# Kernel optimization log

Hardware: AMD Instinct MI355X
Metric: run time of the kernel (lower is better)

The kernel has to match this reference:

```python
import jax, jax.numpy as jnp
import numpy as np

N_NODES = 30000
N_EDGES = 150000
N_REL = 10
IN_DIM = 256
OUT_DIM = 256


def setup_inputs() -> dict:
    key = jax.random.key(0)
    ks = jax.random.split(key, 10)
    s = 1.0 / np.sqrt(IN_DIM)  # ~nn.Linear init scale
    return {
        "x": jax.random.normal(ks[0], (N_NODES, IN_DIM), jnp.float32),
        "W_self": jax.random.uniform(ks[1], (IN_DIM, OUT_DIM), jnp.float32, -s, s),
        "b_self": jax.random.uniform(ks[2], (OUT_DIM,), jnp.float32, -s, s),
        "W_fwd": jax.random.uniform(ks[3], (N_REL, IN_DIM, OUT_DIM), jnp.float32, -s, s),
        "b_fwd": jax.random.uniform(ks[4], (N_REL, OUT_DIM), jnp.float32, -s, s),
        "W_rev": jax.random.uniform(ks[5], (N_REL, IN_DIM, OUT_DIM), jnp.float32, -s, s),
        "b_rev": jax.random.uniform(ks[6], (N_REL, OUT_DIM), jnp.float32, -s, s),
        "dep_idx": jax.random.randint(ks[7], (N_EDGES,), 0, N_NODES, jnp.int32),
        "rel_idx": jax.random.randint(ks[8], (N_EDGES,), 0, N_REL, jnp.int32),
        "gov_idx": jax.random.randint(ks[9], (N_EDGES,), 0, N_NODES, jnp.int32),
    }


def reference(x, W_self, b_self, W_fwd, b_fwd, W_rev, b_rev, dep_idx, rel_idx, gov_idx):
    # self transform for every token: [N, out]
    out = x @ W_self + b_self
    # transform all nodes by every relation weight up-front: [R, N, out]
    H_fwd = jnp.einsum("ni,rio->rno", x, W_fwd) + b_fwd[:, None, :]
    H_rev = jnp.einsum("ni,rio->rno", x, W_rev) + b_rev[:, None, :]
    # per-edge gather: forward msg uses governor feature, reverse msg uses dependent
    msg_fwd = H_fwd[rel_idx, gov_idx]  # [E, out]
    msg_rev = H_rev[rel_idx, dep_idx]  # [E, out]
    # scatter-add: forward msg -> dependent, reverse msg -> governor
    out = out.at[dep_idx].add(msg_fwd)
    out = out.at[gov_idx].add(msg_rev)
    return out
```

## Files before the change

### kernel.cpp

```cpp
#include <hip/hip_runtime.h>

#define N_NODES 30000
#define N_EDGES 150000
#define N_REL 10
#define DIM 256

#define SORT_BLOCKS 120
#define SORT_CHUNK ((N_EDGES + SORT_BLOCKS - 1) / SORT_BLOCKS)

#define SCAN_CHUNK 256
#define SCAN_BLOCKS ((N_NODES + SCAN_CHUNK - 1) / SCAN_CHUNK)

#define PREP_XB 7500
#define PREP_WT 1344

typedef __attribute__((ext_vector_type(8))) short bf16x8;
typedef __attribute__((ext_vector_type(4))) float f32x4;

__device__ __forceinline__ unsigned short f2bf(float f) {
  union { float f; unsigned int u; } v; v.f = f;
  unsigned int u = v.u;
  unsigned int r = u + 0x7fffu + ((u >> 16) & 1u);
  return (unsigned short)(r >> 16);
}


__global__ void prep_hist_kernel(const float* __restrict__ x,
                                 const float* __restrict__ Wf,
                                 const float* __restrict__ Wr,
                                 const float* __restrict__ Ws,
                                 const int* __restrict__ rel,
                                 const int* __restrict__ dep,
                                 const int* __restrict__ gov,
                                 unsigned short* __restrict__ xbf,
                                 unsigned short* __restrict__ wt,
                                 int* __restrict__ block_counts,
                                 int* __restrict__ cnt) {
  int b = blockIdx.x;
  if (b < PREP_XB) {
    int idx = b * 256 + threadIdx.x;
    float4 v = reinterpret_cast<const float4*>(x)[idx];
    ushort4 o;
    o.x = f2bf(v.x); o.y = f2bf(v.y); o.z = f2bf(v.z); o.w = f2bf(v.w);
    reinterpret_cast<ushort4*>(xbf)[idx] = o;
  } else if (b < PREP_XB + PREP_WT) {
    int wb = b - PREP_XB;
    int bb = wb >> 6;
    int tile = wb & 63;
    int ib = tile >> 3, ob = tile & 7;
    const float* src = (bb < N_REL) ? (Wf + (size_t)bb * 65536)
                     : (bb < 2 * N_REL) ? (Wr + (size_t)(bb - N_REL) * 65536)
                     : Ws;
    __shared__ unsigned short tile_s[32][33];
    int c = threadIdx.x & 31, r0 = threadIdx.x >> 5;
    #pragma unroll
    for (int k = 0; k < 4; ++k) {
      int rr = r0 + k * 8;
      tile_s[rr][c] = f2bf(src[(ib * 32 + rr) * 256 + ob * 32 + c]);
    }
    __syncthreads();
    #pragma unroll
    for (int k = 0; k < 4; ++k) {
      int rr = r0 + k * 8;
      wt[(size_t)bb * 65536 + (ob * 32 + rr) * 256 + ib * 32 + c] =
          tile_s[c][rr];
    }
  } else {
    int hb = b - PREP_XB - PREP_WT;
    __shared__ int h[N_REL];
    if (threadIdx.x < N_REL) h[threadIdx.x] = 0;
    __syncthreads();
    int beg = hb * SORT_CHUNK;
    int end = min(beg + SORT_CHUNK, N_EDGES);
    for (int e = beg + threadIdx.x; e < end; e += blockDim.x) {
      atomicAdd(&h[rel[e]], 1);
      atomicAdd(&cnt[dep[e]], 1);
      atomicAdd(&cnt[N_NODES + gov[e]], 1);
    }
    __syncthreads();
    if (threadIdx.x < N_REL)
      block_counts[hb * N_REL + threadIdx.x] = h[threadIdx.x];
  }
}


__global__ void scanA_kernel(const int* __restrict__ cnt,
                             int* __restrict__ tmp, int* __restrict__ sums) {
  __shared__ int s[SCAN_CHUNK];
  int d = blockIdx.y, b = blockIdx.x, t = threadIdx.x;
  int i = b * SCAN_CHUNK + t;
  int v = (i < N_NODES) ? cnt[d * N_NODES + i] : 0;
  s[t] = v;
  __syncthreads();
  for (int off = 1; off < SCAN_CHUNK; off <<= 1) {
    int add = (t >= off) ? s[t - off] : 0;
    __syncthreads();
    s[t] += add;
    __syncthreads();
  }
  if (i < N_NODES) tmp[d * N_NODES + i] = s[t] - v;
  if (t == SCAN_CHUNK - 1) sums[d * SCAN_BLOCKS + b] = s[t];
}


__global__ void scan_finish_kernel(const int* __restrict__ sums,
                                   const int* __restrict__ tmp,
                                   const int* __restrict__ block_counts,
                                   int* __restrict__ rp,
                                   int* __restrict__ cursor,
                                   int* __restrict__ rel_start,
                                   int* __restrict__ block_offset) {
  int d = blockIdx.y, b = blockIdx.x, t = threadIdx.x;

  if (b == SCAN_BLOCKS) {
    if (d == 1) return;
    __shared__ int tot[N_REL];
    __shared__ int rstart[N_REL + 1];
    int r = t;
    if (r < N_REL) {
      int s = 0;
      for (int bb = 0; bb < SORT_BLOCKS; ++bb) s += block_counts[bb * N_REL + r];
      tot[r] = s;
    }
    __syncthreads();
    if (t == 0) {
      int s = 0;
      for (int i = 0; i < N_REL; ++i) { rstart[i] = s; s += tot[i]; }
      rstart[N_REL] = s;
      for (int i = 0; i <= N_REL; ++i) rel_start[i] = rstart[i];
    }
    __syncthreads();
    if (r < N_REL) {
      int run = rstart[r];
      for (int bb = 0; bb < SORT_BLOCKS; ++bb) {
        block_offset[bb * N_REL + r] = run;
        run += block_counts[bb * N_REL + r];
      }
    }
    return;
  }

  __shared__ int ssum[SCAN_BLOCKS];
  __shared__ int spre[SCAN_BLOCKS + 1];
  if (t < SCAN_BLOCKS) ssum[t] = sums[d * SCAN_BLOCKS + t];
  __syncthreads();
  if (t == 0) {
    int run = 0;
    for (int i = 0; i < SCAN_BLOCKS; ++i) { spre[i] = run; run += ssum[i]; }
    spre[SCAN_BLOCKS] = run;
  }
  __syncthreads();
  int chunk = spre[b];
  int i = b * SCAN_CHUNK + t;
  if (i < N_NODES) {
    int v = tmp[d * N_NODES + i] + chunk;
    rp[d * (N_NODES + 1) + i] = v;
    cursor[d * N_NODES + i] = v;
  }
  if (b == 0 && t == 0) rp[d * (N_NODES + 1) + N_NODES] = spre[SCAN_BLOCKS];
}


__global__ void scatter_all_kernel(const int* __restrict__ rel,
                                   const int* __restrict__ dep,
                                   const int* __restrict__ gov,
                                   const int* __restrict__ block_offset,
                                   int* __restrict__ cursor,
                                   int* __restrict__ perm,
                                   int* __restrict__ srcf,
                                   int* __restrict__ srcr,
                                   int* __restrict__ colf,
                                   int* __restrict__ colr) {
  __shared__ int cur[N_REL];
  if (threadIdx.x < N_REL)
    cur[threadIdx.x] = block_offset[blockIdx.x * N_REL + threadIdx.x];
  __syncthreads();
  int beg = blockIdx.x * SORT_CHUNK;
  int end = min(beg + SORT_CHUNK, N_EDGES);
  for (int e = beg + threadIdx.x; e < end; e += blockDim.x) {
    int dp = dep[e], gv = gov[e];
    int pos = atomicAdd(&cur[rel[e]], 1);
    perm[pos] = e;
    srcf[pos] = gv;
    srcr[pos] = dp;
    colf[atomicAdd(&cursor[dp], 1)] = pos;
    colr[atomicAdd(&cursor[N_NODES + gv], 1)] = pos;
  }
}


__global__ __launch_bounds__(256, 2)
void mega_gemm_kernel(const unsigned short* __restrict__ xbf,
                      const unsigned short* __restrict__ wt,
                      const float* __restrict__ b_self,
                      const float* __restrict__ b_fwd,
                      const float* __restrict__ b_rev,
                      const int* __restrict__ srcf,
                      const int* __restrict__ srcr,
                      const int* __restrict__ rel_start,
                      unsigned short* __restrict__ msg,
                      float* __restrict__ out) {
  const int bkt = blockIdx.y;
  const bool is_self = (bkt >= 2 * N_REL);
  const bool fwd = bkt < N_REL;
  const int r = is_self ? 0 : (fwd ? bkt : bkt - N_REL);

  int beg, cnt;
  const int* src_arr = fwd ? srcf : srcr;
  unsigned short* mdir = msg + (fwd ? 0 : (size_t)N_EDGES * DIM);
  if (is_self) {
    beg = (bkt - 2 * N_REL) * (N_NODES / 2);
    cnt = N_NODES / 2;
  } else {
    beg = rel_start[r];
    cnt = rel_start[r + 1] - beg;
  }
  const int ntiles = (cnt + 63) >> 6;
  const int GX = gridDim.x;

  const int tid = threadIdx.x;
  const int wave = tid >> 6, lane = tid & 63;
  const int lm = lane & 15, q = lane >> 4;
  const int nb = wave * 64;
  const int half = lane >> 5;

  __shared__ int s_src[2][64];
  __shared__ unsigned short sA[2][64 * DIM];

  bf16x8 wf[8][4];
  const unsigned short* wbase =
      wt + (size_t)(is_self ? 2 * N_REL : bkt) * DIM * DIM;
  #pragma unroll
  for (int kk = 0; kk < 8; ++kk)
    #pragma unroll
    for (int ni = 0; ni < 4; ++ni)
      wf[kk][ni] = *reinterpret_cast<const bf16x8*>(
          wbase + (size_t)(nb + ni * 16 + lm) * DIM + kk * 32 + q * 8);

  const float* bptr = is_self ? b_self : ((fwd ? b_fwd : b_rev) + r * DIM);
  float bias[4];
  #pragma unroll
  for (int ni = 0; ni < 4; ++ni) bias[ni] = bptr[nb + ni * 16 + lm];

  int swz[8];
  #pragma unroll
  for (int i = 0; i < 8; ++i)
    swz[i] = (((lane & 31) ^ ((i * 2 + half) & 7)) * 8);
  int rowoff[4];
  #pragma unroll
  for (int mi = 0; mi < 4; ++mi) rowoff[mi] = (mi * 16 + lm) * DIM;
  int ckoff[8];
  #pragma unroll
  for (int kk = 0; kk < 8; ++kk)
    ckoff[kk] = ((kk * 4 + q) ^ (lm & 7)) * 8;

  int t = blockIdx.x;
  if (t >= ntiles) return;

  auto load_idx = [&](int tt) -> int {
    int tile0_ = tt << 6;
    if (is_self) {
      int rr = beg + tile0_ + tid;
      return rr < beg + cnt ? rr : beg + cnt - 1;
    } else {
      int p_ = tile0_ + tid;
      p_ = p_ < cnt ? p_ : cnt - 1;
      return src_arr[beg + p_];
    }
  };

  auto issue_stage = [&](int p) {
    const int* sp = s_src[p];
    unsigned short* db = sA[p];
    #pragma unroll
    for (int i = 0; i < 8; ++i) {
      int ldsrow = wave * 16 + i * 2;
      int rr = sp[ldsrow + half];
      const unsigned short* g = xbf + (size_t)rr * DIM + swz[i];
      __builtin_amdgcn_global_load_lds(
          (const __attribute__((address_space(1))) void*)g,
          (__attribute__((address_space(3))) void*)(db + ldsrow * DIM),
          16, 0, 0);
    }
  };

  auto step = [&](int cur) {
    const int tile0 = t << 6;
    const int rows_valid = min(64, cnt - tile0);
    const bool have_next = (t + GX) < ntiles;
    const bool have_next2 = (t + 2 * GX) < ntiles;

    __syncthreads();
    if (have_next) issue_stage(cur ^ 1);
    if (tid < 64 && have_next2) s_src[cur][tid] = load_idx(t + 2 * GX);

    const unsigned short* sAb = sA[cur];
    #pragma unroll
    for (int mi = 0; mi < 4; ++mi) {
      bf16x8 a[8];
      #pragma unroll
      for (int kk = 0; kk < 8; ++kk)
        a[kk] = *reinterpret_cast<const bf16x8*>(sAb + rowoff[mi] + ckoff[kk]);

      f32x4 acc[4];
      #pragma unroll
      for (int ni = 0; ni < 4; ++ni) acc[ni] = (f32x4){0.f, 0.f, 0.f, 0.f};

      __builtin_amdgcn_s_setprio(1);
      #pragma unroll
      for (int kk = 0; kk < 8; ++kk)
        #pragma unroll
        for (int ni = 0; ni < 4; ++ni)
          acc[ni] = __builtin_amdgcn_mfma_f32_16x16x32_bf16(
              a[kk], wf[kk][ni], acc[ni], 0, 0, 0);
      __builtin_amdgcn_s_setprio(0);

      if (is_self) {
        #pragma unroll
        for (int reg = 0; reg < 4; ++reg) {
          int row = mi * 16 + q * 4 + reg;
          if (row < rows_valid) {
            #pragma unroll
            for (int ni = 0; ni < 4; ++ni)
              out[(size_t)(beg + tile0 + row) * DIM + nb + ni * 16 + lm] =
                  acc[ni][reg] + bias[ni];
          }
        }
      } else {
        #pragma unroll
        for (int reg = 0; reg < 4; ++reg) {
          int row = mi * 16 + q * 4 + reg;
          if (row < rows_valid) {
            unsigned int p0 = ((unsigned int)f2bf(acc[1][reg] + bias[1]) << 16) |
                              f2bf(acc[0][reg] + bias[0]);
            unsigned int p1 = ((unsigned int)f2bf(acc[3][reg] + bias[3]) << 16) |
                              f2bf(acc[2][reg] + bias[2]);
            uint2 u; u.x = p0; u.y = p1;
            *reinterpret_cast<uint2*>(
                mdir + (size_t)(beg + tile0 + row) * DIM + nb + lm * 4) = u;
          }
        }
      }
    }
  };

  if (tid < 64) s_src[0][tid] = load_idx(t);
  __syncthreads();
  issue_stage(0);
  if (tid < 64 && t + GX < ntiles) s_src[1][tid] = load_idx(t + GX);

  while (true) {
    step(0);
    t += GX; if (t >= ntiles) break;
    step(1);
    t += GX; if (t >= ntiles) break;
  }
}


__global__ void reduce_both_kernel(const unsigned short* __restrict__ msg,
                                   const int* __restrict__ rp,
                                   const int* __restrict__ colf,
                                   const int* __restrict__ colr,
                                   float* __restrict__ out) {
  const int n = blockIdx.x * 4 + (threadIdx.x >> 6);
  if (n >= N_NODES) return;
  const int lane = threadIdx.x & 63;
  const int b0 = rp[n], e0 = rp[n + 1];
  const int b1 = rp[(N_NODES + 1) + n], e1 = rp[(N_NODES + 1) + n + 1];
  if (e0 == b0 && e1 == b1) return;

  const unsigned short* mrev = msg + (size_t)N_EDGES * DIM;
  float a0 = 0.f, a1 = 0.f, a2 = 0.f, a3 = 0.f;
  union { unsigned int u; float f; } c;

  auto accum = [&](unsigned long long v) {
    unsigned int lo = (unsigned int)v;
    unsigned int hi = (unsigned int)(v >> 32);
    c.u = lo << 16;          a0 += c.f;
    c.u = lo & 0xffff0000u;  a1 += c.f;
    c.u = hi << 16;          a2 += c.f;
    c.u = hi & 0xffff0000u;  a3 += c.f;
  };
  auto ldf = [&](int j) -> unsigned long long {
    return __builtin_nontemporal_load(
        reinterpret_cast<const unsigned long long*>(
            msg + (size_t)colf[j] * DIM + lane * 4));
  };
  auto ldr = [&](int j) -> unsigned long long {
    return __builtin_nontemporal_load(
        reinterpret_cast<const unsigned long long*>(
            mrev + (size_t)colr[j] * DIM + lane * 4));
  };

  int j0 = b0, j1 = b1;
  while (j0 + 1 < e0 && j1 + 1 < e1) {
    unsigned long long v0 = ldf(j0), v1 = ldf(j0 + 1);
    unsigned long long v2 = ldr(j1), v3 = ldr(j1 + 1);
    accum(v0); accum(v1); accum(v2); accum(v3);
    j0 += 2; j1 += 2;
  }
  for (; j0 + 1 < e0; j0 += 2) {
    unsigned long long v0 = ldf(j0), v1 = ldf(j0 + 1);
    accum(v0); accum(v1);
  }
  if (j0 < e0) accum(ldf(j0));
  for (; j1 + 1 < e1; j1 += 2) {
    unsigned long long v0 = ldr(j1), v1 = ldr(j1 + 1);
    accum(v0); accum(v1);
  }
  if (j1 < e1) accum(ldr(j1));

  const int cb = (lane >> 4) * 64 + (lane & 15);
  float* op = out + (size_t)n * DIM;
  op[cb +  0] += a0;
  op[cb + 16] += a1;
  op[cb + 32] += a2;
  op[cb + 48] += a3;
}


__global__ __launch_bounds__(256, 2)
void self_gemm_kernel(const unsigned short* __restrict__ xbf,
                      const unsigned short* __restrict__ wt_self,
                      const float* __restrict__ b_self,
                      float* __restrict__ out) {
  const int tid = threadIdx.x;
  const int wave = tid >> 6, lane = tid & 63;
  const int lm = lane & 15, q = lane >> 4;
  const int nb = wave * 64;

  bf16x8 wf[8][4];
  #pragma unroll
  for (int kk = 0; kk < 8; ++kk)
    #pragma unroll
    for (int ni = 0; ni < 4; ++ni)
      wf[kk][ni] = *reinterpret_cast<const bf16x8*>(
          wt_self + (size_t)(nb + ni * 16 + lm) * DIM + kk * 32 + q * 8);

  float bias[4];
  #pragma unroll
  for (int ni = 0; ni < 4; ++ni) bias[ni] = b_self[nb + ni * 16 + lm];

  const int ntiles = (N_NODES + 63) / 64;
  for (int t = blockIdx.x; t < ntiles; t += gridDim.x) {
    const int row0 = t * 64;
    const unsigned short* xr[4];
    #pragma unroll
    for (int mi = 0; mi < 4; ++mi) {
      int r = row0 + mi * 16 + lm;
      int rc = r < N_NODES ? r : N_NODES - 1;
      xr[mi] = xbf + (size_t)rc * DIM + q * 8;
    }

    f32x4 acc[4][4];
    #pragma unroll
    for (int mi = 0; mi < 4; ++mi)
      #pragma unroll
      for (int ni = 0; ni < 4; ++ni)
        acc[mi][ni] = (f32x4){0.f, 0.f, 0.f, 0.f};

    #pragma unroll
    for (int kk = 0; kk < 8; ++kk) {
      bf16x8 a[4];
      #pragma unroll
      for (int mi = 0; mi < 4; ++mi)
        a[mi] = *reinterpret_cast<const bf16x8*>(xr[mi] + kk * 32);
      #pragma unroll
      for (int mi = 0; mi < 4; ++mi)
        #pragma unroll
        for (int ni = 0; ni < 4; ++ni)
          acc[mi][ni] = __builtin_amdgcn_mfma_f32_16x16x32_bf16(a[mi], wf[kk][ni], acc[mi][ni], 0, 0, 0);
    }

    #pragma unroll
    for (int mi = 0; mi < 4; ++mi) {
      #pragma unroll
      for (int reg = 0; reg < 4; ++reg) {
        int row = row0 + mi * 16 + q * 4 + reg;
        if (row < N_NODES) {
          #pragma unroll
          for (int ni = 0; ni < 4; ++ni)
            out[(size_t)row * DIM + nb + ni * 16 + lm] = acc[mi][ni][reg] + bias[ni];
        }
      }
    }
  }
}

__global__ void edge_gemm_atomic_kernel(const unsigned short* __restrict__ xbf,
                                        const unsigned short* __restrict__ wt,
                                        const float* __restrict__ b_fwd,
                                        const float* __restrict__ b_rev,
                                        const int* __restrict__ perm,
                                        const int* __restrict__ rel_start,
                                        const int* __restrict__ dep,
                                        const int* __restrict__ gov,
                                        float* __restrict__ out) {
  const int bucket = blockIdx.y;
  const int r = bucket % N_REL;
  const bool fwd = bucket < N_REL;
  const int beg = rel_start[r];
  const int cnt = rel_start[r + 1] - beg;
  const int ntiles = (cnt + 63) >> 6;

  const int tid = threadIdx.x;
  const int wave = tid >> 6, lane = tid & 63;
  const int lm = lane & 15, q = lane >> 4;
  const int nb = wave * 64;

  __shared__ int s_src[64], s_dst[64];

  const unsigned short* wr[4];
  #pragma unroll
  for (int ni = 0; ni < 4; ++ni)
    wr[ni] = wt + (size_t)bucket * DIM * DIM + (size_t)(nb + ni * 16 + lm) * DIM + q * 8;

  const float* bptr = (fwd ? b_fwd : b_rev) + r * DIM;
  float bias[4];
  #pragma unroll
  for (int ni = 0; ni < 4; ++ni) bias[ni] = bptr[nb + ni * 16 + lm];

  for (int t = blockIdx.x; t < ntiles; t += gridDim.x) {
    const int tile0 = t << 6;
    const int rows_valid = min(64, cnt - tile0);

    if (tid < 64) {
      int s = 0, d = -1;
      if (tid < rows_valid) {
        int e = perm[beg + tile0 + tid];
        int gv = gov[e], dp = dep[e];
        s = fwd ? gv : dp;
        d = fwd ? dp : gv;
      }
      s_src[tid] = s;
      s_dst[tid] = d;
    }
    __syncthreads();

    const unsigned short* xr[4];
    #pragma unroll
    for (int mi = 0; mi < 4; ++mi)
      xr[mi] = xbf + (size_t)s_src[mi * 16 + lm] * DIM + q * 8;

    f32x4 acc[4][4];
    #pragma unroll
    for (int mi = 0; mi < 4; ++mi)
      #pragma unroll
      for (int ni = 0; ni < 4; ++ni)
        acc[mi][ni] = (f32x4){0.f, 0.f, 0.f, 0.f};

    #pragma unroll
    for (int k0 = 0; k0 < DIM; k0 += 32) {
      bf16x8 a[4], b[4];
      #pragma unroll
      for (int mi = 0; mi < 4; ++mi) a[mi] = *reinterpret_cast<const bf16x8*>(xr[mi] + k0);
      #pragma unroll
      for (int ni = 0; ni < 4; ++ni) b[ni] = *reinterpret_cast<const bf16x8*>(wr[ni] + k0);
      #pragma unroll
      for (int mi = 0; mi < 4; ++mi)
        #pragma unroll
        for (int ni = 0; ni < 4; ++ni)
          acc[mi][ni] = __builtin_amdgcn_mfma_f32_16x16x32_bf16(a[mi], b[ni], acc[mi][ni], 0, 0, 0);
    }

    #pragma unroll
    for (int mi = 0; mi < 4; ++mi) {
      #pragma unroll
      for (int reg = 0; reg < 4; ++reg) {
        int row = mi * 16 + q * 4 + reg;
        if (row < rows_valid) {
          int dst = s_dst[row];
          float* op = out + (size_t)dst * DIM + nb + lm;
          #pragma unroll
          for (int ni = 0; ni < 4; ++ni)
            atomicAdd(op + ni * 16, acc[mi][ni][reg] + bias[ni]);
        }
      }
    }
    __syncthreads();
  }
}


extern "C" void kernel_launch(void* const* d_in, const int* in_sizes, int n_in,
                              void* d_out, int out_size, void* d_ws, size_t ws_size,
                              hipStream_t stream) {
  const float* x      = (const float*)d_in[0];
  const float* W_self = (const float*)d_in[1];
  const float* b_self = (const float*)d_in[2];
  const float* W_fwd  = (const float*)d_in[3];
  const float* b_fwd  = (const float*)d_in[4];
  const float* W_rev  = (const float*)d_in[5];
  const float* b_rev  = (const float*)d_in[6];
  const int* dep = (const int*)d_in[7];
  const int* rel = (const int*)d_in[8];
  const int* gov = (const int*)d_in[9];
  float* out = (float*)d_out;

  char* base = (char*)d_ws;
  size_t off = 0;
  auto alloc = [&](size_t bytes) -> char* {
    char* p = base + off;
    off = (off + bytes + 15) & ~(size_t)15;
    return p;
  };

  unsigned short* xbf = (unsigned short*)alloc((size_t)N_NODES * DIM * 2);
  unsigned short* wt  = (unsigned short*)alloc((size_t)21 * DIM * DIM * 2);
  int* perm          = (int*)alloc((size_t)N_EDGES * 4);
  int* srcf          = (int*)alloc((size_t)N_EDGES * 4);
  int* srcr          = (int*)alloc((size_t)N_EDGES * 4);
  int* rel_start     = (int*)alloc(16 * 4);
  int* block_counts  = (int*)alloc(SORT_BLOCKS * N_REL * 4);
  int* block_offset  = (int*)alloc(SORT_BLOCKS * N_REL * 4);
  int* cnt       = (int*)alloc((size_t)2 * N_NODES * 4);
  int* tmp       = (int*)alloc((size_t)2 * N_NODES * 4);
  int* sums      = (int*)alloc((size_t)2 * SCAN_BLOCKS * 4);
  int* rp        = (int*)alloc((size_t)2 * (N_NODES + 1) * 4);
  int* cursor    = (int*)alloc((size_t)2 * N_NODES * 4);
  int* colf      = (int*)alloc((size_t)N_EDGES * 4);
  int* colr      = (int*)alloc((size_t)N_EDGES * 4);
  unsigned short* msg = (unsigned short*)alloc((size_t)2 * N_EDGES * DIM * 2);
  const bool two_phase = (off <= ws_size);

  hipMemsetAsync(cnt, 0, (size_t)2 * N_NODES * 4, stream);
  prep_hist_kernel<<<PREP_XB + PREP_WT + SORT_BLOCKS, 256, 0, stream>>>(
      x, W_fwd, W_rev, W_self, rel, dep, gov, xbf, wt, block_counts, cnt);
  scanA_kernel<<<dim3(SCAN_BLOCKS, 2), SCAN_CHUNK, 0, stream>>>(cnt, tmp, sums);
  scan_finish_kernel<<<dim3(SCAN_BLOCKS + 1, 2), SCAN_CHUNK, 0, stream>>>(
      sums, tmp, block_counts, rp, cursor, rel_start, block_offset);
  scatter_all_kernel<<<SORT_BLOCKS, 256, 0, stream>>>(
      rel, dep, gov, block_offset, cursor, perm, srcf, srcr, colf, colr);

  if (two_phase) {
    mega_gemm_kernel<<<dim3(48, 2 * N_REL + 2), 256, 0, stream>>>(
        xbf, wt, b_self, b_fwd, b_rev, srcf, srcr, rel_start, msg, out);
    reduce_both_kernel<<<(N_NODES + 3) / 4, 256, 0, stream>>>(
        msg, rp, colf, colr, out);
  } else {
    self_gemm_kernel<<<120, 256, 0, stream>>>(
        xbf, wt + (size_t)20 * DIM * DIM, b_self, out);
    edge_gemm_atomic_kernel<<<dim3(260, 20), 256, 0, stream>>>(
        xbf, wt, b_fwd, b_rev, perm, rel_start, dep, gov, out);
  }
}
```

Measured before the change: 279.4 us.

## Drop double-buffered gather pipeline for single LDS buffer and higher occupancy

Replaces the two-stage software pipeline, where the next tile's row gather overlapped the current tile's MFMA work, with a single-buffered loop: load indices, sync, gather rows into LDS, sync, compute. This halves the LDS footprint per block and raises the launch-bounds occupancy hint from 2 to 4 blocks, so overlap is meant to come from more resident waves instead of in-block prefetching. The risk is that each thread keeps the whole weight tile in registers (about 128 VGPRs), so the tighter register budget at 4 blocks could force spills. Losing the explicit prefetch also exposes the gather latency inside each block.

```diff
diff --git a/kernel.cpp b/kernel.cpp
--- a/kernel.cpp
+++ b/kernel.cpp
@@ -189,7 +189,7 @@
 }
 
 
-__global__ __launch_bounds__(256, 2)
+__global__ __launch_bounds__(256, 4)
 void mega_gemm_kernel(const unsigned short* __restrict__ xbf,
                       const unsigned short* __restrict__ wt,
                       const float* __restrict__ b_self,
@@ -224,8 +224,8 @@
   const int nb = wave * 64;
   const int half = lane >> 5;
 
-  __shared__ int s_src[2][64];
-  __shared__ unsigned short sA[2][64 * DIM];
+  __shared__ int s_src[64];
+  __shared__ unsigned short sA[64 * DIM];
 
   bf16x8 wf[8][4];
   const unsigned short* wbase =
@@ -254,53 +254,42 @@
   for (int kk = 0; kk < 8; ++kk)
     ckoff[kk] = ((kk * 4 + q) ^ (lm & 7)) * 8;
 
-  int t = blockIdx.x;
-  if (t >= ntiles) return;
-
-  auto load_idx = [&](int tt) -> int {
-    int tile0_ = tt << 6;
-    if (is_self) {
-      int rr = beg + tile0_ + tid;
-      return rr < beg + cnt ? rr : beg + cnt - 1;
-    } else {
-      int p_ = tile0_ + tid;
-      p_ = p_ < cnt ? p_ : cnt - 1;
-      return src_arr[beg + p_];
-    }
-  };
-
-  auto issue_stage = [&](int p) {
-    const int* sp = s_src[p];
-    unsigned short* db = sA[p];
+  for (int t = blockIdx.x; t < ntiles; t += GX) {
+    const int tile0 = t << 6;
+    const int rows_valid = min(64, cnt - tile0);
+
+    if (tid < 64) {
+      int s;
+      if (is_self) {
+        int rr = beg + tile0 + tid;
+        s = rr < beg + cnt ? rr : beg + cnt - 1;
+      } else {
+        int p_ = tile0 + tid;
+        p_ = p_ < cnt ? p_ : cnt - 1;
+        s = src_arr[beg + p_];
+      }
+      s_src[tid] = s;
+    }
+    __syncthreads();
+
     #pragma unroll
     for (int i = 0; i < 8; ++i) {
       int ldsrow = wave * 16 + i * 2;
-      int rr = sp[ldsrow + half];
+      int rr = s_src[ldsrow + half];
       const unsigned short* g = xbf + (size_t)rr * DIM + swz[i];
       __builtin_amdgcn_global_load_lds(
           (const __attribute__((address_space(1))) void*)g,
-          (__attribute__((address_space(3))) void*)(db + ldsrow * DIM),
+          (__attribute__((address_space(3))) void*)(sA + ldsrow * DIM),
           16, 0, 0);
     }
-  };
-
-  auto step = [&](int cur) {
-    const int tile0 = t << 6;
-    const int rows_valid = min(64, cnt - tile0);
-    const bool have_next = (t + GX) < ntiles;
-    const bool have_next2 = (t + 2 * GX) < ntiles;
-
-    __syncthreads();
-    if (have_next) issue_stage(cur ^ 1);
-    if (tid < 64 && have_next2) s_src[cur][tid] = load_idx(t + 2 * GX);
-
-    const unsigned short* sAb = sA[cur];
+    __syncthreads();
+
     #pragma unroll
     for (int mi = 0; mi < 4; ++mi) {
       bf16x8 a[8];
       #pragma unroll
       for (int kk = 0; kk < 8; ++kk)
-        a[kk] = *reinterpret_cast<const bf16x8*>(sAb + rowoff[mi] + ckoff[kk]);
+        a[kk] = *reinterpret_cast<const bf16x8*>(sA + rowoff[mi] + ckoff[kk]);
 
       f32x4 acc[4];
       #pragma unroll
@@ -342,18 +331,6 @@
         }
       }
     }
-  };
-
-  if (tid < 64) s_src[0][tid] = load_idx(t);
-  __syncthreads();
-  issue_stage(0);
-  if (tid < 64 && t + GX < ntiles) s_src[1][tid] = load_idx(t + GX);
-
-  while (true) {
-    step(0);
-    t += GX; if (t >= ntiles) break;
-    step(1);
-    t += GX; if (t >= ntiles) break;
   }
 }
 
```

New measurement: 515.7 us. 84.6% more time.
